# Kernel tuning notes

Measured on AMD Instinct MI355X. Metric: run time of the kernel, lower is better.

The kernel has to match this reference:

```python
import jax, jax.numpy as jnp
import numpy as np

EMB = 1024
NUM_HEADS = 16


def setup_inputs() -> dict:
    key = jax.random.key(0)
    k_x, k_k, k_q, k_v, k_u, k_b = jax.random.split(key, 6)
    b, s, e = 4, 2048, EMB
    lim = 1.0 / np.sqrt(e)
    return {
        "x": jax.random.normal(k_x, (b, s, e), dtype=jnp.float32),
        "Wk": jax.random.uniform(k_k, (e, e), jnp.float32, -lim, lim),
        "Wq": jax.random.uniform(k_q, (e, e), jnp.float32, -lim, lim),
        "Wv": jax.random.uniform(k_v, (e, e), jnp.float32, -lim, lim),
        "Wu": jax.random.uniform(k_u, (e, e), jnp.float32, -lim, lim),
        "bu": jax.random.uniform(k_b, (e,), jnp.float32, -lim, lim),
    }


def reference(x, Wk, Wq, Wv, Wu, bu):
    b, s, e = x.shape
    h = NUM_HEADS
    d = e // h
    # scale q and k each by emb**(-1/4), as in the original (note: emb, not head_size)
    scale = e ** -0.25
    # project and split heads: (b, h, s, d)
    q = (x @ Wq.T).reshape(b, s, h, d).transpose(0, 2, 1, 3) * scale
    k = (x @ Wk.T).reshape(b, s, h, d).transpose(0, 2, 1, 3) * scale
    v = (x @ Wv.T).reshape(b, s, h, d).transpose(0, 2, 1, 3)
    # attention scores (b, h, s, s)
    dot = jnp.einsum("bhqd,bhkd->bhqk", q, k)
    # causal mask: strictly-upper triangle (offset=1) set to -inf
    causal = jnp.triu(jnp.ones((s, s), dtype=bool), k=1)
    dot = jnp.where(causal[None, None, :, :], -jnp.inf, dot)
    attn = jax.nn.softmax(dot, axis=-1)
    out = jnp.einsum("bhqk,bhkd->bhqd", attn, v)
    out = out.transpose(0, 2, 1, 3).reshape(b, s, e)
    return out @ Wu.T + bu
```

## Files before the change

### kernel.cpp

```cpp
#include <hip/hip_runtime.h>
#include <stdint.h>
#include <math.h>


typedef __attribute__((ext_vector_type(8))) short bf16x8;
typedef __attribute__((ext_vector_type(4))) float f32x4;
typedef __attribute__((ext_vector_type(16))) float f32x16;
typedef __attribute__((ext_vector_type(4))) int i32x4;
typedef __attribute__((ext_vector_type(4))) short s16x4;

#define GLOAD_LDS16(gp, lp)                                                     \
  __builtin_amdgcn_global_load_lds(                                             \
      (__attribute__((address_space(1))) void*)(gp),                            \
      (__attribute__((address_space(3))) void*)(lp), 16, 0, 0)

#define WAITVM(N) asm volatile("s_waitcnt vmcnt(" #N ")" ::: "memory")

__device__ __forceinline__ short f2bf(float f) {
  union { float f; uint32_t u; } v; v.f = f;
  uint32_t r = v.u + 0x7FFFu + ((v.u >> 16) & 1u);
  return (short)(r >> 16);
}
__device__ __forceinline__ float bf2f(short s) {
  union { uint32_t u; float f; } v; v.u = ((uint32_t)(uint16_t)s) << 16;
  return v.f;
}
__device__ __forceinline__ short f2bfn(float f) {
  union { __bf16 h; short s; } u; u.h = (__bf16)f; return u.s;
}
__device__ __forceinline__ uint32_t pk2n(float a, float b) {
  union { __bf16 h[2]; uint32_t u; } v;
  v.h[0] = (__bf16)a; v.h[1] = (__bf16)b;
  return v.u;
}

__device__ __forceinline__ void swap32(uint32_t a, uint32_t b, int hi,
                                       uint32_t& out0, uint32_t& out1) {
#if __has_builtin(__builtin_amdgcn_permlane32_swap)
  typedef __attribute__((ext_vector_type(2))) int i32x2;
  i32x2 r = __builtin_amdgcn_permlane32_swap((int)a, (int)b, false, false);
  out0 = (uint32_t)r.x; out1 = (uint32_t)r.y;
#else
  uint32_t ta = (uint32_t)__shfl_xor((int)a, 32);
  uint32_t tb = (uint32_t)__shfl_xor((int)b, 32);
  out0 = hi ? tb : a;
  out1 = hi ? b : ta;
#endif
}

__global__ __launch_bounds__(256) void cast_kernel(const float* __restrict__ src,
                                                   short* __restrict__ dst, int n) {
  int i = (blockIdx.x * 256 + threadIdx.x) * 8;
  if (i >= n) return;
  const float4* s = (const float4*)(src + i);
  float4 f0 = s[0], f1 = s[1];
  bf16x8 o;
  o[0] = f2bf(f0.x); o[1] = f2bf(f0.y); o[2] = f2bf(f0.z); o[3] = f2bf(f0.w);
  o[4] = f2bf(f1.x); o[5] = f2bf(f1.y); o[6] = f2bf(f1.z); o[7] = f2bf(f1.w);
  *(bf16x8*)(dst + i) = o;
}

__global__ __launch_bounds__(256) void cast4_kernel(const float* __restrict__ w0,
                                                    const float* __restrict__ w1,
                                                    const float* __restrict__ w2,
                                                    const float* __restrict__ w3,
                                                    short* o0, short* o1, short* o2, short* o3) {
  const float* src = (blockIdx.y == 0) ? w0 : (blockIdx.y == 1) ? w1 : (blockIdx.y == 2) ? w2 : w3;
  short* dst = (blockIdx.y == 0) ? o0 : (blockIdx.y == 1) ? o1 : (blockIdx.y == 2) ? o2 : o3;
  int i = (blockIdx.x * 256 + threadIdx.x) * 8;
  const float4* s = (const float4*)(src + i);
  float4 f0 = s[0], f1 = s[1];
  bf16x8 o;
  o[0] = f2bf(f0.x); o[1] = f2bf(f0.y); o[2] = f2bf(f0.z); o[3] = f2bf(f0.w);
  o[4] = f2bf(f1.x); o[5] = f2bf(f1.y); o[6] = f2bf(f1.z); o[7] = f2bf(f1.w);
  *(bf16x8*)(dst + i) = o;
}

template <bool F32OUT>
__device__ __forceinline__ void gemm_bt_core(const short* __restrict__ A,
                                             const short* __restrict__ Bm,
                                             short* __restrict__ Cb,
                                             float* __restrict__ Cf,
                                             const float* __restrict__ bias) {
  __shared__ short a_lds[128 * 64];
  __shared__ short b_lds[128 * 64];
  const int tid = threadIdx.x;
  const int w = tid >> 6, l = tid & 63;
  const int l15 = l & 15, lhi = l >> 4;
  const int wr = w >> 1, wc = w & 1;
  const int row0 = blockIdx.x * 128;
  const int col0 = blockIdx.y * 128;

  f32x4 acc[4][4];
#pragma unroll
  for (int m = 0; m < 4; ++m)
#pragma unroll
    for (int n = 0; n < 4; ++n)
      acc[m][n] = (f32x4){0.f, 0.f, 0.f, 0.f};

  const int o0 = tid * 16;
  const int sr = o0 >> 7;
  const int sc = o0 & 127;

  for (int kt = 0; kt < 16; ++kt) {
    const char* Ab = (const char*)A + (size_t)(row0 + sr) * 2048 + kt * 128 + sc;
    const char* Bb = (const char*)Bm + (size_t)(col0 + sr) * 2048 + kt * 128 + sc;
#pragma unroll
    for (int i = 0; i < 4; ++i) {
      GLOAD_LDS16(Ab + (size_t)i * 32 * 2048, (char*)a_lds + i * 4096 + o0);
      GLOAD_LDS16(Bb + (size_t)i * 32 * 2048, (char*)b_lds + i * 4096 + o0);
    }
    __syncthreads();
#pragma unroll
    for (int kk = 0; kk < 2; ++kk) {
      bf16x8 af[4], bg[4];
#pragma unroll
      for (int m = 0; m < 4; ++m) {
        int r = wr * 64 + m * 16 + l15;
        af[m] = *(const bf16x8*)((const char*)a_lds + r * 128 + kk * 64 + lhi * 16);
      }
#pragma unroll
      for (int n = 0; n < 4; ++n) {
        int r = wc * 64 + n * 16 + l15;
        bg[n] = *(const bf16x8*)((const char*)b_lds + r * 128 + kk * 64 + lhi * 16);
      }
#pragma unroll
      for (int m = 0; m < 4; ++m)
#pragma unroll
        for (int n = 0; n < 4; ++n)
          acc[m][n] = __builtin_amdgcn_mfma_f32_16x16x32_bf16(af[m], bg[n], acc[m][n], 0, 0, 0);
    }
    __syncthreads();
  }

#pragma unroll
  for (int m = 0; m < 4; ++m) {
#pragma unroll
    for (int n = 0; n < 4; ++n) {
      int colg = col0 + wc * 64 + n * 16 + l15;
#pragma unroll
      for (int r = 0; r < 4; ++r) {
        int rowg = row0 + wr * 64 + m * 16 + lhi * 4 + r;
        float v = acc[m][n][r];
        if constexpr (F32OUT) {
          Cf[(size_t)rowg * 1024 + colg] = v + bias[colg];
        } else {
          Cb[(size_t)rowg * 1024 + colg] = f2bfn(v);
        }
      }
    }
  }
}

__global__ __launch_bounds__(256) void gemm_qkv_kernel(const short* __restrict__ xb,
                                                       const short* __restrict__ wq,
                                                       const short* __restrict__ wk,
                                                       const short* __restrict__ wv,
                                                       short* qo, short* ko, short* vo) {
  const short* Bm = (blockIdx.z == 0) ? wq : (blockIdx.z == 1) ? wk : wv;
  short* C = (blockIdx.z == 0) ? qo : (blockIdx.z == 1) ? ko : vo;
  gemm_bt_core<false>(xb, Bm, C, nullptr, nullptr);
}

__global__ __launch_bounds__(256) void gemm_out_kernel(const short* __restrict__ ob,
                                                       const short* __restrict__ wu,
                                                       const float* __restrict__ bias,
                                                       float* __restrict__ out) {
  gemm_bt_core<true>(ob, wu, nullptr, out, bias);
}

__global__ __launch_bounds__(256) void frag_qk_kernel(const short* __restrict__ qb,
                                                      const short* __restrict__ kb,
                                                      short* __restrict__ qf,
                                                      short* __restrict__ kf) {
  int t = blockIdx.x, bh = blockIdx.y;
  int b = bh >> 4, h = bh & 15;
  __shared__ short q_t[32][72], k_t[32][72];
  int tid = threadIdx.x;
  int row = tid >> 3, seg = tid & 7;
  size_t src = ((size_t)(b * 2048 + t * 32 + row)) * 1024 + h * 64 + seg * 8;
  *(bf16x8*)&q_t[row][seg * 8] = *(const bf16x8*)(qb + src);
  *(bf16x8*)&k_t[row][seg * 8] = *(const bf16x8*)(kb + src);
  __syncthreads();
  int s = tid >> 6, l = tid & 63, l31 = l & 31, hi = l >> 5;
  bf16x8 cq = *(const bf16x8*)&q_t[l31][hi * 8 + s * 16];
  bf16x8 ck = *(const bf16x8*)&k_t[l31][hi * 8 + s * 16];
  size_t dst = ((size_t)bh * 64 + t) * 2048 + s * 512 + l * 8;
  *(bf16x8*)(qf + dst) = cq;
  *(bf16x8*)(kf + dst) = ck;
}

__global__ __launch_bounds__(256) void frag_v_kernel(const short* __restrict__ vb,
                                                     short* __restrict__ vf) {
  int t = blockIdx.x, bh = blockIdx.y;
  int b = bh >> 4, h = bh & 15;
  __shared__ short v_t[32][72];
  int tid = threadIdx.x;
  int row = tid >> 3, seg = tid & 7;
  *(bf16x8*)&v_t[row][seg * 8] =
      *(const bf16x8*)(vb + ((size_t)(b * 2048 + t * 32 + row)) * 1024 + h * 64 + seg * 8);
  __syncthreads();
  int u = tid >> 6, l = tid & 63, l31 = l & 31, hi = l >> 5;
  int dblk = u >> 1, koff = u & 1;
  bf16x8 c;
#pragma unroll
  for (int j = 0; j < 8; ++j) c[j] = v_t[koff * 16 + hi * 8 + j][dblk * 32 + l31];
  *(bf16x8*)(vf + ((size_t)bh * 64 + t) * 2048 + u * 512 + l * 8) = c;
}

__global__ __launch_bounds__(512) void attn_kernel(const short* __restrict__ qf,
                                                   const short* __restrict__ kf,
                                                   const short* __restrict__ vf,
                                                   short* __restrict__ ob) {
  const float QSCALE = 0.03125f * 1.44269504f;
  int id = blockIdx.x;
  int p = id >> 6;
  int bh = id & 63;
  int b = bh >> 4, h = bh & 15;
  int tid = threadIdx.x;
  int wid = tid >> 6, l = tid & 63;
  int l31 = l & 31, hi = l >> 5;
  int qs = wid & 3, team = wid >> 2;

  __shared__ short kbuf[2][4096];
  __shared__ short vbuf[2][4096];
  __shared__ float mrg[4][64][34];

  const short* qfb = qf + (size_t)bh * 131072;
  const short* kfb = kf + (size_t)bh * 131072;
  const short* vfb = vf + (size_t)bh * 131072;

  bf16x8 ones;
#pragma unroll
  for (int j = 0; j < 8; ++j) ones[j] = (short)0x3F80;

#define STAGE(t, bi) do {                                                  \
    GLOAD_LDS16(kfb + (size_t)(t) * 4096 + tid * 8,                        \
                (char*)&kbuf[bi][0] + tid * 16);                           \
    GLOAD_LDS16(vfb + (size_t)(t) * 4096 + tid * 8,                        \
                (char*)&vbuf[bi][0] + tid * 16);                           \
  } while (0)

  for (int part = 0; part < 2; ++part) {
    int j = part ? (15 - p) : p;
    int qt = 4 * j + qs;
    int qrow0 = qt * 32;
    int qg = qrow0 + l31;
    int qmax = qrow0 + 31;
    int nk = 2 * (j + 1);

    bf16x8 aq[4];
    {
      const short* qp = qfb + qt * 2048 + l * 8;
#pragma unroll
      for (int s = 0; s < 4; ++s) {
        bf16x8 t = *(const bf16x8*)(qp + s * 512);
#pragma unroll
        for (int jj = 0; jj < 8; ++jj) t[jj] = f2bfn(bf2f(t[jj]) * QSCALE);
        aq[s] = t;
      }
    }

    f32x16 o_lo = {}, o_hi = {}, o_sum = {};

    STAGE(0, 0);
    STAGE(1, 1);
    WAITVM(2);
    __builtin_amdgcn_s_barrier();
    __builtin_amdgcn_sched_barrier(0);

    for (int t = 0; t < nk; ++t) {
      int cur = t & 1;
      int k0w = t * 64 + team * 32;
      if (k0w <= qmax) {
        const char* kb_ = (const char*)&kbuf[cur][0] + team * 4096;
        const char* vb_ = (const char*)&vbuf[cur][0] + team * 4096;
        f32x16 st;
#pragma unroll
        for (int r = 0; r < 16; ++r) st[r] = -8.0f;
#pragma unroll
        for (int s = 0; s < 4; ++s) {
          bf16x8 ak = *(const bf16x8*)(kb_ + (s * 64 + l) * 16);
          st = __builtin_amdgcn_mfma_f32_32x32x16_bf16(ak, aq[s], st, 0, 0, 0);
        }

        if (k0w + 31 > qrow0) {
#pragma unroll
          for (int r = 0; r < 16; ++r) {
            int kk = k0w + (r & 3) + 8 * (r >> 2) + 4 * hi;
            if (kk > qg) st[r] = -INFINITY;
          }
        }

#pragma unroll
        for (int r = 0; r < 16; ++r) st[r] = exp2f(st[r]);

        uint32_t a0, a2, b1, b3, c0, c2, d1, d3;
        swap32(pk2n(st[0], st[1]),   pk2n(st[4], st[5]),   hi, a0, a2);
        swap32(pk2n(st[2], st[3]),   pk2n(st[6], st[7]),   hi, b1, b3);
        swap32(pk2n(st[8], st[9]),   pk2n(st[12], st[13]), hi, c0, c2);
        swap32(pk2n(st[10], st[11]), pk2n(st[14], st[15]), hi, d1, d3);
        i32x4 u0 = {(int)a0, (int)b1, (int)a2, (int)b3};
        i32x4 u1 = {(int)c0, (int)d1, (int)c2, (int)d3};
        bf16x8 pa0 = __builtin_bit_cast(bf16x8, u0);
        bf16x8 pa1 = __builtin_bit_cast(bf16x8, u1);

        bf16x8 av;
        av = *(const bf16x8*)(vb_ + (0 * 64 + l) * 16);
        o_lo = __builtin_amdgcn_mfma_f32_32x32x16_bf16(av, pa0, o_lo, 0, 0, 0);
        av = *(const bf16x8*)(vb_ + (1 * 64 + l) * 16);
        o_lo = __builtin_amdgcn_mfma_f32_32x32x16_bf16(av, pa1, o_lo, 0, 0, 0);
        av = *(const bf16x8*)(vb_ + (2 * 64 + l) * 16);
        o_hi = __builtin_amdgcn_mfma_f32_32x32x16_bf16(av, pa0, o_hi, 0, 0, 0);
        av = *(const bf16x8*)(vb_ + (3 * 64 + l) * 16);
        o_hi = __builtin_amdgcn_mfma_f32_32x32x16_bf16(av, pa1, o_hi, 0, 0, 0);
        o_sum = __builtin_amdgcn_mfma_f32_32x32x16_bf16(ones, pa0, o_sum, 0, 0, 0);
        o_sum = __builtin_amdgcn_mfma_f32_32x32x16_bf16(ones, pa1, o_sum, 0, 0, 0);
      }
      __builtin_amdgcn_s_barrier();
      __builtin_amdgcn_sched_barrier(0);
      if (t + 2 < nk) {
        STAGE(t + 2, cur);
        WAITVM(2);
      } else {
        WAITVM(0);
      }
      __builtin_amdgcn_s_barrier();
      __builtin_amdgcn_sched_barrier(0);
    }

    float lsum = o_sum[0];
    if (team == 1) {
      float* pp = &mrg[qs][l][0];
#pragma unroll
      for (int r = 0; r < 16; ++r) { pp[r] = o_lo[r]; pp[16 + r] = o_hi[r]; }
      pp[32] = lsum;
    }
    __syncthreads();
    if (team == 0) {
      const float* pp = &mrg[qs][l][0];
      float inv = 1.0f / (lsum + pp[32]);
      short* obase = ob + (size_t)(b * 2048 + qg) * 1024 + h * 64;
#pragma unroll
      for (int g = 0; g < 4; ++g) {
        int d0 = 8 * g + 4 * hi;
        s16x4 v0, v1;
#pragma unroll
        for (int jj = 0; jj < 4; ++jj) {
          v0[jj] = f2bfn((o_lo[4 * g + jj] + pp[4 * g + jj]) * inv);
          v1[jj] = f2bfn((o_hi[4 * g + jj] + pp[16 + 4 * g + jj]) * inv);
        }
        *(s16x4*)(obase + d0) = v0;
        *(s16x4*)(obase + 32 + d0) = v1;
      }
    }
    __syncthreads();
  }
#undef STAGE
}

extern "C" void kernel_launch(void* const* d_in, const int* in_sizes, int n_in,
                              void* d_out, int out_size, void* d_ws, size_t ws_size,
                              hipStream_t stream) {
  const float* x  = (const float*)d_in[0];
  const float* Wk = (const float*)d_in[1];
  const float* Wq = (const float*)d_in[2];
  const float* Wv = (const float*)d_in[3];
  const float* Wu = (const float*)d_in[4];
  const float* bu = (const float*)d_in[5];
  float* out = (float*)d_out;

  char* ws = (char*)d_ws;
  const size_t MB = 1u << 20;
  short* xb  = (short*)(ws + 0 * MB);
  short* qf  = (short*)(ws + 0 * MB);
  short* qb  = (short*)(ws + 16 * MB);
  short* vfb = (short*)(ws + 16 * MB);
  short* kb  = (short*)(ws + 32 * MB);
  short* vb  = (short*)(ws + 48 * MB);
  short* kfb = (short*)(ws + 64 * MB);
  short* ob  = (short*)(ws + 80 * MB);
  short* wqb = (short*)(ws + 96 * MB);
  short* wkb = (short*)(ws + 98 * MB);
  short* wvb = (short*)(ws + 100 * MB);
  short* wub = (short*)(ws + 102 * MB);

  cast_kernel<<<4096, 256, 0, stream>>>(x, xb, 8388608);
  cast4_kernel<<<dim3(512, 4), 256, 0, stream>>>(Wq, Wk, Wv, Wu, wqb, wkb, wvb, wub);

  gemm_qkv_kernel<<<dim3(64, 8, 3), 256, 0, stream>>>(xb, wqb, wkb, wvb, qb, kb, vb);
  frag_qk_kernel<<<dim3(64, 64), 256, 0, stream>>>(qb, kb, qf, kfb);
  frag_v_kernel<<<dim3(64, 64), 256, 0, stream>>>(vb, vfb);
  attn_kernel<<<512, 512, 0, stream>>>(qf, kfb, vfb, ob);
  gemm_out_kernel<<<dim3(64, 8), 256, 0, stream>>>(ob, wub, bu, out);
}
```

Baseline: 211.1 us.

## Load K/V fragments directly from global memory, split keys across wave pairs

Drops the double-buffered LDS staging of K/V tiles and the per-iteration block barriers. Each wave now reads K and V fragments straight from global memory (relying on L2/L1) and owns one 32-row query tile, with two waves splitting the key range in half. The row sum moves from an extra MFMA against a ones vector to a VALU reduction plus a cross-half shuffle. The trade is more global/cache traffic and exposed load latency against less synchronisation and LDS use, and the per-wave key work becomes less balanced.

```diff
diff --git a/kernel.cpp b/kernel.cpp
--- a/kernel.cpp
+++ b/kernel.cpp
@@ -13,8 +13,6 @@
   __builtin_amdgcn_global_load_lds(                                             \
       (__attribute__((address_space(1))) void*)(gp),                            \
       (__attribute__((address_space(3))) void*)(lp), 16, 0, 0)
-
-#define WAITVM(N) asm volatile("s_waitcnt vmcnt(" #N ")" ::: "memory")
 
 __device__ __forceinline__ short f2bf(float f) {
   union { float f; uint32_t u; } v; v.f = f;
@@ -213,45 +211,32 @@
                                                    const short* __restrict__ vf,
                                                    short* __restrict__ ob) {
   const float QSCALE = 0.03125f * 1.44269504f;
-  int id = blockIdx.x;
-  int p = id >> 6;
-  int bh = id & 63;
+  int bh = blockIdx.x;
   int b = bh >> 4, h = bh & 15;
   int tid = threadIdx.x;
   int wid = tid >> 6, l = tid & 63;
   int l31 = l & 31, hi = l >> 5;
-  int qs = wid & 3, team = wid >> 2;
-
-  __shared__ short kbuf[2][4096];
-  __shared__ short vbuf[2][4096];
+  int pair = blockIdx.y * 4 + (wid >> 1);
+  int team = wid & 1;
+  int slot = wid >> 1;
+
   __shared__ float mrg[4][64][34];
 
   const short* qfb = qf + (size_t)bh * 131072;
   const short* kfb = kf + (size_t)bh * 131072;
   const short* vfb = vf + (size_t)bh * 131072;
 
-  bf16x8 ones;
-#pragma unroll
-  for (int j = 0; j < 8; ++j) ones[j] = (short)0x3F80;
-
-#define STAGE(t, bi) do {                                                  \
-    GLOAD_LDS16(kfb + (size_t)(t) * 4096 + tid * 8,                        \
-                (char*)&kbuf[bi][0] + tid * 16);                           \
-    GLOAD_LDS16(vfb + (size_t)(t) * 4096 + tid * 8,                        \
-                (char*)&vbuf[bi][0] + tid * 16);                           \
-  } while (0)
-
   for (int part = 0; part < 2; ++part) {
-    int j = part ? (15 - p) : p;
-    int qt = 4 * j + qs;
-    int qrow0 = qt * 32;
+    int sidx = part ? (63 - pair) : pair;
+    int qrow0 = sidx * 32;
     int qg = qrow0 + l31;
-    int qmax = qrow0 + 31;
-    int nk = 2 * (j + 1);
+    int n = sidx + 1;
+    int t0 = team ? (n >> 1) : 0;
+    int t1 = team ? n : (n >> 1);
 
     bf16x8 aq[4];
     {
-      const short* qp = qfb + qt * 2048 + l * 8;
+      const short* qp = qfb + sidx * 2048 + l * 8;
 #pragma unroll
       for (int s = 0; s < 4; ++s) {
         bf16x8 t = *(const bf16x8*)(qp + s * 512);
@@ -261,84 +246,71 @@
       }
     }
 
-    f32x16 o_lo = {}, o_hi = {}, o_sum = {};
-
-    STAGE(0, 0);
-    STAGE(1, 1);
-    WAITVM(2);
-    __builtin_amdgcn_s_barrier();
-    __builtin_amdgcn_sched_barrier(0);
-
-    for (int t = 0; t < nk; ++t) {
-      int cur = t & 1;
-      int k0w = t * 64 + team * 32;
-      if (k0w <= qmax) {
-        const char* kb_ = (const char*)&kbuf[cur][0] + team * 4096;
-        const char* vb_ = (const char*)&vbuf[cur][0] + team * 4096;
-        f32x16 st;
-#pragma unroll
-        for (int r = 0; r < 16; ++r) st[r] = -8.0f;
-#pragma unroll
-        for (int s = 0; s < 4; ++s) {
-          bf16x8 ak = *(const bf16x8*)(kb_ + (s * 64 + l) * 16);
-          st = __builtin_amdgcn_mfma_f32_32x32x16_bf16(ak, aq[s], st, 0, 0, 0);
+    f32x16 o_lo = {}, o_hi = {};
+    float lsum = 0.f;
+
+    for (int t = t0; t < t1; ++t) {
+      const short* kp = kfb + (size_t)t * 2048 + l * 8;
+      const short* vp = vfb + (size_t)t * 2048 + l * 8;
+      f32x16 st;
+#pragma unroll
+      for (int r = 0; r < 16; ++r) st[r] = -8.0f;
+#pragma unroll
+      for (int s = 0; s < 4; ++s) {
+        bf16x8 ak = *(const bf16x8*)(kp + s * 512);
+        st = __builtin_amdgcn_mfma_f32_32x32x16_bf16(ak, aq[s], st, 0, 0, 0);
+      }
+
+      if (t == sidx) {
+#pragma unroll
+        for (int r = 0; r < 16; ++r) {
+          int kk = qrow0 + (r & 3) + 8 * (r >> 2) + 4 * hi;
+          if (kk > qg) st[r] = -INFINITY;
         }
-
-        if (k0w + 31 > qrow0) {
-#pragma unroll
-          for (int r = 0; r < 16; ++r) {
-            int kk = k0w + (r & 3) + 8 * (r >> 2) + 4 * hi;
-            if (kk > qg) st[r] = -INFINITY;
-          }
-        }
-
-#pragma unroll
-        for (int r = 0; r < 16; ++r) st[r] = exp2f(st[r]);
-
-        uint32_t a0, a2, b1, b3, c0, c2, d1, d3;
-        swap32(pk2n(st[0], st[1]),   pk2n(st[4], st[5]),   hi, a0, a2);
-        swap32(pk2n(st[2], st[3]),   pk2n(st[6], st[7]),   hi, b1, b3);
-        swap32(pk2n(st[8], st[9]),   pk2n(st[12], st[13]), hi, c0, c2);
-        swap32(pk2n(st[10], st[11]), pk2n(st[14], st[15]), hi, d1, d3);
-        i32x4 u0 = {(int)a0, (int)b1, (int)a2, (int)b3};
-        i32x4 u1 = {(int)c0, (int)d1, (int)c2, (int)d3};
-        bf16x8 pa0 = __builtin_bit_cast(bf16x8, u0);
-        bf16x8 pa1 = __builtin_bit_cast(bf16x8, u1);
-
-        bf16x8 av;
-        av = *(const bf16x8*)(vb_ + (0 * 64 + l) * 16);
-        o_lo = __builtin_amdgcn_mfma_f32_32x32x16_bf16(av, pa0, o_lo, 0, 0, 0);
-        av = *(const bf16x8*)(vb_ + (1 * 64 + l) * 16);
-        o_lo = __builtin_amdgcn_mfma_f32_32x32x16_bf16(av, pa1, o_lo, 0, 0, 0);
-        av = *(const bf16x8*)(vb_ + (2 * 64 + l) * 16);
-        o_hi = __builtin_amdgcn_mfma_f32_32x32x16_bf16(av, pa0, o_hi, 0, 0, 0);
-        av = *(const bf16x8*)(vb_ + (3 * 64 + l) * 16);
-        o_hi = __builtin_amdgcn_mfma_f32_32x32x16_bf16(av, pa1, o_hi, 0, 0, 0);
-        o_sum = __builtin_amdgcn_mfma_f32_32x32x16_bf16(ones, pa0, o_sum, 0, 0, 0);
-        o_sum = __builtin_amdgcn_mfma_f32_32x32x16_bf16(ones, pa1, o_sum, 0, 0, 0);
-      }
-      __builtin_amdgcn_s_barrier();
-      __builtin_amdgcn_sched_barrier(0);
-      if (t + 2 < nk) {
-        STAGE(t + 2, cur);
-        WAITVM(2);
-      } else {
-        WAITVM(0);
-      }
-      __builtin_amdgcn_s_barrier();
-      __builtin_amdgcn_sched_barrier(0);
-    }
-
-    float lsum = o_sum[0];
+      }
+
+#pragma unroll
+      for (int r = 0; r < 16; ++r) st[r] = exp2f(st[r]);
+
+      float sm[8];
+#pragma unroll
+      for (int r = 0; r < 8; ++r) sm[r] = st[r] + st[r + 8];
+#pragma unroll
+      for (int r = 0; r < 4; ++r) sm[r] += sm[r + 4];
+      lsum += (sm[0] + sm[1]) + (sm[2] + sm[3]);
+
+      uint32_t a0, a2, b1, b3, c0, c2, d1, d3;
+      swap32(pk2n(st[0], st[1]),   pk2n(st[4], st[5]),   hi, a0, a2);
+      swap32(pk2n(st[2], st[3]),   pk2n(st[6], st[7]),   hi, b1, b3);
+      swap32(pk2n(st[8], st[9]),   pk2n(st[12], st[13]), hi, c0, c2);
+      swap32(pk2n(st[10], st[11]), pk2n(st[14], st[15]), hi, d1, d3);
+      i32x4 u0 = {(int)a0, (int)b1, (int)a2, (int)b3};
+      i32x4 u1 = {(int)c0, (int)d1, (int)c2, (int)d3};
+      bf16x8 pa0 = __builtin_bit_cast(bf16x8, u0);
+      bf16x8 pa1 = __builtin_bit_cast(bf16x8, u1);
+
+      bf16x8 av;
+      av = *(const bf16x8*)(vp);
+      o_lo = __builtin_amdgcn_mfma_f32_32x32x16_bf16(av, pa0, o_lo, 0, 0, 0);
+      av = *(const bf16x8*)(vp + 512);
+      o_lo = __builtin_amdgcn_mfma_f32_32x32x16_bf16(av, pa1, o_lo, 0, 0, 0);
+      av = *(const bf16x8*)(vp + 1024);
+      o_hi = __builtin_amdgcn_mfma_f32_32x32x16_bf16(av, pa0, o_hi, 0, 0, 0);
+      av = *(const bf16x8*)(vp + 1536);
+      o_hi = __builtin_amdgcn_mfma_f32_32x32x16_bf16(av, pa1, o_hi, 0, 0, 0);
+    }
+
+    lsum += __shfl_xor(lsum, 32);
+
     if (team == 1) {
-      float* pp = &mrg[qs][l][0];
+      float* pp = &mrg[slot][l][0];
 #pragma unroll
       for (int r = 0; r < 16; ++r) { pp[r] = o_lo[r]; pp[16 + r] = o_hi[r]; }
       pp[32] = lsum;
     }
     __syncthreads();
     if (team == 0) {
-      const float* pp = &mrg[qs][l][0];
+      const float* pp = &mrg[slot][l][0];
       float inv = 1.0f / (lsum + pp[32]);
       short* obase = ob + (size_t)(b * 2048 + qg) * 1024 + h * 64;
 #pragma unroll
@@ -356,7 +328,6 @@
     }
     __syncthreads();
   }
-#undef STAGE
 }
 
 extern "C" void kernel_launch(void* const* d_in, const int* in_sizes, int n_in,
@@ -391,6 +362,6 @@
   gemm_qkv_kernel<<<dim3(64, 8, 3), 256, 0, stream>>>(xb, wqb, wkb, wvb, qb, kb, vb);
   frag_qk_kernel<<<dim3(64, 64), 256, 0, stream>>>(qb, kb, qf, kfb);
   frag_v_kernel<<<dim3(64, 64), 256, 0, stream>>>(vb, vfb);
-  attn_kernel<<<512, 512, 0, stream>>>(qf, kfb, vfb, ob);
+  attn_kernel<<<dim3(64, 8), 512, 0, stream>>>(qf, kfb, vfb, ob);
   gemm_out_kernel<<<dim3(64, 8), 256, 0, stream>>>(ob, wub, bu, out);
 }
```

After: 198.3 us. -6.1%, faster.
